# Kernel optimization log

Hardware: AMD Instinct MI355X
Metric: run time of the kernel (lower is better)

The kernel has to match this reference:

```python
import jax, jax.numpy as jnp
import numpy as np

N_POINTS = 1048576
N_LEVELS = 16
F = 2
BASE_RES = 16
FINEST_RES = 512
LOG2_HASH = 19
SIZES = [2 ** min(i + 1, LOG2_HASH) for i in range(N_LEVELS)]  # per-level table rows (powers of 2)
OFFS = np.concatenate([[0], np.cumsum(SIZES)]).astype(np.int64)  # static row offsets into packed table
TOTAL_ROWS = int(OFFS[-1])  # 131070
# hash primes from the torch module; uint32 wraparound matches int64 low-bit behavior
# because each table size is a power of two <= 2^19 < 2^32, so h % 2^k == low k bits.
P0, P1, P2, P3 = np.uint32(1), np.uint32(2654435761), np.uint32(29675113), np.uint32(123456789)
CORNERS = np.array([[0,0,0],[1,0,0],[0,1,0],[1,1,0],
                    [0,0,1],[1,0,1],[0,1,1],[1,1,1]], dtype=np.uint32)  # torch stacking order


def setup_inputs() -> dict:
    key = jax.random.key(0)
    k1, k2 = jax.random.split(key)
    coords = jax.random.uniform(k1, (N_POINTS, 3), dtype=jnp.float32, minval=-1.0, maxval=1.0)
    hash_init_scale = 0.001
    table = jax.random.uniform(k2, (TOTAL_ROWS, F), dtype=jnp.float32,
                               minval=-hash_init_scale, maxval=hash_init_scale)
    return {"coords": coords, "table": table}


def _encode(coords, table):
    corners = jnp.asarray(CORNERS)  # [8,3] uint32
    outs = []
    for level in range(N_LEVELS):
        res = min(BASE_RES * (2 ** level), FINEST_RES)
        cs = (coords + 1.0) * res           # [N,3]
        cf = jnp.floor(cs)
        frac = cs - cf                      # [N,3]
        base = cf.astype(jnp.uint32)        # coords >= -1 so floor >= 0
        c = base[None, :, :] + corners[:, None, :]   # [8,N,3]
        x, y, z = c[..., 0], c[..., 1], c[..., 2]
        h = x * P0
        h = h * P1 + y
        h = h * P2 + z
        h = h * P3
        h = (h & jnp.uint32(SIZES[level] - 1)).astype(jnp.int32)  # mod power-of-2 table size
        feats = table[int(OFFS[level]) + h]          # [8,N,F] gather
        tx = frac[..., 0:1]; ty = frac[..., 1:2]; tz = frac[..., 2:3]
        f = (feats[0] * (1 - tx) * (1 - ty) * (1 - tz)
             + feats[1] * tx * (1 - ty) * (1 - tz)
             + feats[2] * (1 - tx) * ty * (1 - tz)
             + feats[3] * tx * ty * (1 - tz)
             + feats[4] * (1 - tx) * (1 - ty) * tz
             + feats[5] * tx * (1 - ty) * tz
             + feats[6] * (1 - tx) * ty * tz
             + feats[7] * tx * ty * tz)              # [N,F]
        outs.append(f)
    return jnp.concatenate(outs, axis=-1)            # [N, N_LEVELS*F]


def reference(coords, table):
    return _encode(coords, table)
```

## Files before the change

### kernel.cpp

```cpp
#include <hip/hip_runtime.h>
#include <hip/hip_fp16.h>


#define BLOCK 1024
#define NBLOCKS 512
#define ITERS 16
#define STAGED_ROWS 16382
#define TBL_LDS_BYTES 65536
#define LDS_BYTES (TBL_LDS_BYTES + 16 * 128 * 8)

__device__ __forceinline__ float2 ldsRow(const unsigned* lds, unsigned idx) {
    unsigned u = lds[idx];
    __half2 h = *(__half2*)&u;
    return __half22float2(h);
}

#define PREP(FRES, HARR, WARR) \
    unsigned HARR[8]; float WARR[8]; { \
        const float csx = (px + 1.0f) * (FRES); \
        const float csy = (py + 1.0f) * (FRES); \
        const float csz = (pz + 1.0f) * (FRES); \
        const float cfx = floorf(csx), cfy = floorf(csy), cfz = floorf(csz); \
        const float tx = csx - cfx, ty = csy - cfy, tz = csz - cfz; \
        const unsigned hh = (unsigned)cfx * HA + (unsigned)cfy * HB + (unsigned)cfz * HC; \
        const float ux = 1.0f - tx, uy = 1.0f - ty, uz = 1.0f - tz; \
        WARR[0] = ux*uy*uz; WARR[1] = tx*uy*uz; WARR[2] = ux*ty*uz; WARR[3] = tx*ty*uz; \
        WARR[4] = ux*uy*tz; WARR[5] = tx*uy*tz; WARR[6] = ux*ty*tz; WARR[7] = tx*ty*tz; \
        HARR[0] = hh;           HARR[1] = hh + HA;           \
        HARR[2] = hh + HB;      HARR[3] = hh + HA + HB;      \
        HARR[4] = hh + HC;      HARR[5] = hh + HA + HC;      \
        HARR[6] = hh + HB + HC; HARR[7] = hh + HA + HB + HC; \
    }

#define GATHER_LDS(HARR, WARR, MASK, OFF, O0, O1) \
    { _Pragma("unroll") for (int c = 0; c < 8; ++c) { \
        float2 f = ldsRow(lds_tb, (OFF) + ((HARR[c]) & (MASK))); \
        (O0) += f.x * WARR[c]; (O1) += f.y * WARR[c]; } }

#define GATHER_GBL(HARR, WARR, MASK, OFF, O0, O1) \
    { _Pragma("unroll") for (int c = 0; c < 8; ++c) { \
        float2 f = tb[(OFF) + ((HARR[c]) & (MASK))]; \
        (O0) += f.x * WARR[c]; (O1) += f.y * WARR[c]; } }

__global__ __launch_bounds__(BLOCK) void ngp_encode_kernel(
    const float* __restrict__ coords,
    const float* __restrict__ table,
    float* __restrict__ out)
{
    extern __shared__ unsigned char lds_raw[];
    unsigned* lds_tb = (unsigned*)lds_raw;
    float2* lds_t = (float2*)(lds_raw + TBL_LDS_BYTES);

    {
        const float4* __restrict__ t4 = (const float4*)table;
        uint2* __restrict__ l2 = (uint2*)lds_tb;
        for (int r = threadIdx.x; r < STAGED_ROWS / 2; r += BLOCK) {
            float4 v = t4[r];
            __half2 a = __floats2half2_rn(v.x, v.y);
            __half2 b = __floats2half2_rn(v.z, v.w);
            uint2 u;
            u.x = *(unsigned*)&a;
            u.y = *(unsigned*)&b;
            l2[r] = u;
        }
    }
    __syncthreads();

    constexpr unsigned P1 = 2654435761u, P2 = 29675113u, P3 = 123456789u;
    constexpr unsigned HA = P1 * P2 * P3;
    constexpr unsigned HB = P2 * P3;
    constexpr unsigned HC = P3;

    const float2* __restrict__ tb = (const float2*)table;
    float4* __restrict__ out4 = (float4*)out;

    const int wv   = __builtin_amdgcn_readfirstlane((int)(threadIdx.x >> 6));
    const int q    = wv & 7;
    const int g    = wv >> 3;
    const int lane = threadIdx.x & 63;
    const int pl   = g * 64 + lane;

    const int lA = q;
    const int lB = 15 - q;
    const unsigned maskA = (2u << lA) - 1u, offA = maskA - 1u;
    const unsigned maskB = (2u << lB) - 1u, offB = maskB - 1u;

    for (int it = 0; it < ITERS; ++it) {
        const int pbase = blockIdx.x * (ITERS * 128) + it * 128;
        const int p = pbase + pl;

        const float px = coords[3 * p + 0];
        const float py = coords[3 * p + 1];
        const float pz = coords[3 * p + 2];

        float oA0 = 0.0f, oA1 = 0.0f, oB0 = 0.0f, oB1 = 0.0f;

        if (q < 3) {
            {
                PREP(512.0f, hB, wB)
                GATHER_GBL(hB, wB, maskB, offB, oB0, oB1)
            }
            {
                const float fresA = (float)(16 << lA);
                PREP(fresA, hA, wA)
                GATHER_LDS(hA, wA, maskA, offA, oA0, oA1)
            }
        } else if (q < 5) {
            {
                const float fresA = (float)(16 << lA);
                PREP(fresA, hA, wA)
                GATHER_LDS(hA, wA, maskA, offA, oA0, oA1)
            }
            {
                PREP(512.0f, hB, wB)
                GATHER_LDS(hB, wB, maskB, offB, oB0, oB1)
            }
        } else {
            PREP(512.0f, hc, wc)
            GATHER_LDS(hc, wc, maskA, offA, oA0, oA1)
            GATHER_LDS(hc, wc, maskB, offB, oB0, oB1)
        }

        lds_t[lA * 128 + (pl ^ (lA & 14))] = make_float2(oA0, oA1);
        lds_t[lB * 128 + (pl ^ (lB & 14))] = make_float2(oB0, oB1);
        __syncthreads();
        {
            const int j  = threadIdx.x;
            const int lp = j >> 3, qq = j & 7;
            float2 a = lds_t[(2 * qq + 0) * 128 + (lp ^ (2 * qq))];
            float2 b = lds_t[(2 * qq + 1) * 128 + (lp ^ (2 * qq))];
            out4[(size_t)pbase * 8 + j] = make_float4(a.x, a.y, b.x, b.y);
        }
        __syncthreads();
    }
}

extern "C" void kernel_launch(void* const* d_in, const int* in_sizes, int n_in,
                              void* d_out, int out_size, void* d_ws, size_t ws_size,
                              hipStream_t stream) {
    const float* coords = (const float*)d_in[0];
    const float* table  = (const float*)d_in[1];
    float* out = (float*)d_out;

    hipFuncSetAttribute((const void*)ngp_encode_kernel,
                        hipFuncAttributeMaxDynamicSharedMemorySize,
                        LDS_BYTES);

    ngp_encode_kernel<<<NBLOCKS, BLOCK, LDS_BYTES, stream>>>(coords, table, out);
}
```

Baseline: 226.2 us.

## Stage hash table in LDS as fp32 and specialize per-wave level pairs

Stages levels 0-12 of the table in LDS as fp32 instead of converting to fp16 halves, doubling the staged table footprint to 128 KB. This drops the per-lookup half-to-float conversion and the precision loss. Each wave's level pair becomes a compile-time template, so masks and offsets are constants and hashes are pre-scaled to byte offsets. The global gathers for the finest levels are issued before the LDS work to hide their latency. The larger LDS allocation, about 144 KB per 1024-thread block, may limit blocks per CU and makes the staging copy longer.

```diff
diff --git a/kernel.cpp b/kernel.cpp
--- a/kernel.cpp
+++ b/kernel.cpp
@@ -5,42 +5,107 @@
 #define BLOCK 1024
 #define NBLOCKS 512
 #define ITERS 16
-#define STAGED_ROWS 16382
-#define TBL_LDS_BYTES 65536
+#define TBL_ROWS 16382
+#define TBL_LDS_BYTES 131072
 #define LDS_BYTES (TBL_LDS_BYTES + 16 * 128 * 8)
 
-__device__ __forceinline__ float2 ldsRow(const unsigned* lds, unsigned idx) {
-    unsigned u = lds[idx];
-    __half2 h = *(__half2*)&u;
-    return __half22float2(h);
-}
+constexpr unsigned P1 = 2654435761u, P2 = 29675113u, P3 = 123456789u;
+constexpr unsigned HA = P1 * P2 * P3;
+constexpr unsigned HB = P2 * P3;
+constexpr unsigned HC = P3;
 
-#define PREP(FRES, HARR, WARR) \
-    unsigned HARR[8]; float WARR[8]; { \
+#define PREP3(FRES, H3, WARR) \
+    unsigned H3[8]; float WARR[8]; { \
         const float csx = (px + 1.0f) * (FRES); \
         const float csy = (py + 1.0f) * (FRES); \
         const float csz = (pz + 1.0f) * (FRES); \
         const float cfx = floorf(csx), cfy = floorf(csy), cfz = floorf(csz); \
         const float tx = csx - cfx, ty = csy - cfy, tz = csz - cfz; \
-        const unsigned hh = (unsigned)cfx * HA + (unsigned)cfy * HB + (unsigned)cfz * HC; \
+        const unsigned hh = ((unsigned)cfx * HA + (unsigned)cfy * HB + (unsigned)cfz * HC) << 3; \
         const float ux = 1.0f - tx, uy = 1.0f - ty, uz = 1.0f - tz; \
-        WARR[0] = ux*uy*uz; WARR[1] = tx*uy*uz; WARR[2] = ux*ty*uz; WARR[3] = tx*ty*uz; \
-        WARR[4] = ux*uy*tz; WARR[5] = tx*uy*tz; WARR[6] = ux*ty*tz; WARR[7] = tx*ty*tz; \
-        HARR[0] = hh;           HARR[1] = hh + HA;           \
-        HARR[2] = hh + HB;      HARR[3] = hh + HA + HB;      \
-        HARR[4] = hh + HC;      HARR[5] = hh + HA + HC;      \
-        HARR[6] = hh + HB + HC; HARR[7] = hh + HA + HB + HC; \
+        const float m00 = uy * uz, m10 = ty * uz, m01 = uy * tz, m11 = ty * tz; \
+        WARR[0] = ux * m00; WARR[1] = tx * m00; \
+        WARR[2] = ux * m10; WARR[3] = tx * m10; \
+        WARR[4] = ux * m01; WARR[5] = tx * m01; \
+        WARR[6] = ux * m11; WARR[7] = tx * m11; \
+        H3[0] = hh;                        H3[1] = hh + (HA << 3); \
+        H3[2] = hh + (HB << 3);            H3[3] = hh + ((HA + HB) << 3); \
+        H3[4] = hh + (HC << 3);            H3[5] = hh + ((HA + HC) << 3); \
+        H3[6] = hh + ((HB + HC) << 3);     H3[7] = hh + ((HA + HB + HC) << 3); \
     }
 
-#define GATHER_LDS(HARR, WARR, MASK, OFF, O0, O1) \
-    { _Pragma("unroll") for (int c = 0; c < 8; ++c) { \
-        float2 f = ldsRow(lds_tb, (OFF) + ((HARR[c]) & (MASK))); \
-        (O0) += f.x * WARR[c]; (O1) += f.y * WARR[c]; } }
+template<int LA, int LB, bool GB>
+__device__ __forceinline__ void computePair(
+    const char* ldsb, const float* __restrict__ table,
+    float px, float py, float pz, float2& oA, float2& oB)
+{
+    constexpr unsigned MA8 = ((2u << LA) - 1u) << 3;
+    constexpr unsigned OA8 = ((2u << LA) - 2u) << 3;
+    constexpr unsigned MB8 = ((2u << LB) - 1u) << 3;
+    constexpr unsigned OB8 = ((2u << LB) - 2u) << 3;
 
-#define GATHER_GBL(HARR, WARR, MASK, OFF, O0, O1) \
-    { _Pragma("unroll") for (int c = 0; c < 8; ++c) { \
-        float2 f = tb[(OFF) + ((HARR[c]) & (MASK))]; \
-        (O0) += f.x * WARR[c]; (O1) += f.y * WARR[c]; } }
+    float a0 = 0.0f, a1 = 0.0f, b0 = 0.0f, b1 = 0.0f;
+
+    if constexpr (GB) {
+        PREP3(512.0f, h3B, wB)
+        const char* gb = (const char*)table + OB8;
+        const float2 g0 = *(const float2*)(gb + (h3B[0] & MB8));
+        const float2 g1 = *(const float2*)(gb + (h3B[1] & MB8));
+        const float2 g2 = *(const float2*)(gb + (h3B[2] & MB8));
+        const float2 g3 = *(const float2*)(gb + (h3B[3] & MB8));
+        const float2 g4 = *(const float2*)(gb + (h3B[4] & MB8));
+        const float2 g5 = *(const float2*)(gb + (h3B[5] & MB8));
+        const float2 g6 = *(const float2*)(gb + (h3B[6] & MB8));
+        const float2 g7 = *(const float2*)(gb + (h3B[7] & MB8));
+        {
+            PREP3((float)(16 << LA), h3A, wA)
+#pragma unroll
+            for (int c = 0; c < 8; ++c) {
+                float2 f = *(const float2*)(ldsb + OA8 + (h3A[c] & MA8));
+                a0 += f.x * wA[c]; a1 += f.y * wA[c];
+            }
+        }
+        b0 += g0.x * wB[0]; b1 += g0.y * wB[0];
+        b0 += g1.x * wB[1]; b1 += g1.y * wB[1];
+        b0 += g2.x * wB[2]; b1 += g2.y * wB[2];
+        b0 += g3.x * wB[3]; b1 += g3.y * wB[3];
+        b0 += g4.x * wB[4]; b1 += g4.y * wB[4];
+        b0 += g5.x * wB[5]; b1 += g5.y * wB[5];
+        b0 += g6.x * wB[6]; b1 += g6.y * wB[6];
+        b0 += g7.x * wB[7]; b1 += g7.y * wB[7];
+    } else if constexpr (LA >= 5) {
+        PREP3(512.0f, h3, w)
+#pragma unroll
+        for (int c = 0; c < 8; ++c) {
+            float2 f = *(const float2*)(ldsb + OA8 + (h3[c] & MA8));
+            a0 += f.x * w[c]; a1 += f.y * w[c];
+        }
+#pragma unroll
+        for (int c = 0; c < 8; ++c) {
+            float2 f = *(const float2*)(ldsb + OB8 + (h3[c] & MB8));
+            b0 += f.x * w[c]; b1 += f.y * w[c];
+        }
+    } else {
+        {
+            PREP3((float)(16 << LA), h3A, wA)
+#pragma unroll
+            for (int c = 0; c < 8; ++c) {
+                float2 f = *(const float2*)(ldsb + OA8 + (h3A[c] & MA8));
+                a0 += f.x * wA[c]; a1 += f.y * wA[c];
+            }
+        }
+        {
+            PREP3(512.0f, h3B, wB)
+#pragma unroll
+            for (int c = 0; c < 8; ++c) {
+                float2 f = *(const float2*)(ldsb + OB8 + (h3B[c] & MB8));
+                b0 += f.x * wB[c]; b1 += f.y * wB[c];
+            }
+        }
+    }
+    oA = make_float2(a0, a1);
+    oB = make_float2(b0, b1);
+}
 
 __global__ __launch_bounds__(BLOCK) void ngp_encode_kernel(
     const float* __restrict__ coords,
@@ -48,30 +113,19 @@
     float* __restrict__ out)
 {
     extern __shared__ unsigned char lds_raw[];
-    unsigned* lds_tb = (unsigned*)lds_raw;
+    const char* ldsb = (const char*)lds_raw;
     float2* lds_t = (float2*)(lds_raw + TBL_LDS_BYTES);
 
     {
         const float4* __restrict__ t4 = (const float4*)table;
-        uint2* __restrict__ l2 = (uint2*)lds_tb;
-        for (int r = threadIdx.x; r < STAGED_ROWS / 2; r += BLOCK) {
-            float4 v = t4[r];
-            __half2 a = __floats2half2_rn(v.x, v.y);
-            __half2 b = __floats2half2_rn(v.z, v.w);
-            uint2 u;
-            u.x = *(unsigned*)&a;
-            u.y = *(unsigned*)&b;
-            l2[r] = u;
-        }
+        float4* __restrict__ l4 = (float4*)lds_raw;
+        for (int r = threadIdx.x; r < TBL_ROWS / 2; r += BLOCK)
+            l4[r] = t4[r];
     }
     __syncthreads();
 
-    constexpr unsigned P1 = 2654435761u, P2 = 29675113u, P3 = 123456789u;
-    constexpr unsigned HA = P1 * P2 * P3;
-    constexpr unsigned HB = P2 * P3;
-    constexpr unsigned HC = P3;
-
-    const float2* __restrict__ tb = (const float2*)table;
+    const float2* __restrict__ tbf = (const float2*)table;
+    (void)tbf;
     float4* __restrict__ out4 = (float4*)out;
 
     const int wv   = __builtin_amdgcn_readfirstlane((int)(threadIdx.x >> 6));
@@ -82,8 +136,7 @@
 
     const int lA = q;
     const int lB = 15 - q;
-    const unsigned maskA = (2u << lA) - 1u, offA = maskA - 1u;
-    const unsigned maskB = (2u << lB) - 1u, offB = maskB - 1u;
+    const unsigned xA = (unsigned)(lA & 14), xB = (unsigned)(lB & 14);
 
     for (int it = 0; it < ITERS; ++it) {
         const int pbase = blockIdx.x * (ITERS * 128) + it * 128;
@@ -93,36 +146,20 @@
         const float py = coords[3 * p + 1];
         const float pz = coords[3 * p + 2];
 
-        float oA0 = 0.0f, oA1 = 0.0f, oB0 = 0.0f, oB1 = 0.0f;
-
-        if (q < 3) {
-            {
-                PREP(512.0f, hB, wB)
-                GATHER_GBL(hB, wB, maskB, offB, oB0, oB1)
-            }
-            {
-                const float fresA = (float)(16 << lA);
-                PREP(fresA, hA, wA)
-                GATHER_LDS(hA, wA, maskA, offA, oA0, oA1)
-            }
-        } else if (q < 5) {
-            {
-                const float fresA = (float)(16 << lA);
-                PREP(fresA, hA, wA)
-                GATHER_LDS(hA, wA, maskA, offA, oA0, oA1)
-            }
-            {
-                PREP(512.0f, hB, wB)
-                GATHER_LDS(hB, wB, maskB, offB, oB0, oB1)
-            }
-        } else {
-            PREP(512.0f, hc, wc)
-            GATHER_LDS(hc, wc, maskA, offA, oA0, oA1)
-            GATHER_LDS(hc, wc, maskB, offB, oB0, oB1)
+        float2 oA, oB;
+        switch (q) {
+        case 0: computePair<0, 15, true >(ldsb, table, px, py, pz, oA, oB); break;
+        case 1: computePair<1, 14, true >(ldsb, table, px, py, pz, oA, oB); break;
+        case 2: computePair<2, 13, true >(ldsb, table, px, py, pz, oA, oB); break;
+        case 3: computePair<3, 12, false>(ldsb, table, px, py, pz, oA, oB); break;
+        case 4: computePair<4, 11, false>(ldsb, table, px, py, pz, oA, oB); break;
+        case 5: computePair<5, 10, false>(ldsb, table, px, py, pz, oA, oB); break;
+        case 6: computePair<6,  9, false>(ldsb, table, px, py, pz, oA, oB); break;
+        default: computePair<7, 8, false>(ldsb, table, px, py, pz, oA, oB); break;
         }
 
-        lds_t[lA * 128 + (pl ^ (lA & 14))] = make_float2(oA0, oA1);
-        lds_t[lB * 128 + (pl ^ (lB & 14))] = make_float2(oB0, oB1);
+        lds_t[lA * 128 + (pl ^ xA)] = oA;
+        lds_t[lB * 128 + (pl ^ xB)] = oB;
         __syncthreads();
         {
             const int j  = threadIdx.x;
```

After: 248.7 us. +9.9%, slower.
